# Kernel tuning notes

Hardware: AMD Instinct MI355X
Metric: run time of the kernel (lower is better)

Reference implementation:

```python
import jax, jax.numpy as jnp
import numpy as np

N, E, H, S = 50000, 400000, 128, 3  # nodes, edges, hidden_dim, mp steps
NODE_IN, EDGE_IN, OUT = 4, 3, 2


def _mlp(x, W1, b1, W2, b2, W3, b3):
    # MLP(in, [H, H], out): Linear->ReLU->Linear->ReLU->Linear
    h = jax.nn.relu(x @ W1 + b1)
    h = jax.nn.relu(h @ W2 + b2)
    return h @ W3 + b3


def setup_inputs() -> dict:
    key = jax.random.key(0)
    ks = iter(jax.random.split(key, 64))

    def p(shape):
        fan_in = shape[-2]
        return (jax.random.normal(next(ks), shape, jnp.float32) / np.float32(np.sqrt(fan_in)))

    inp = {}
    inp["x"] = jax.random.normal(next(ks), (N, NODE_IN), jnp.float32)
    inp["edge_attr"] = jax.random.normal(next(ks), (E, EDGE_IN), jnp.float32)
    inp["edge_index"] = jax.random.randint(next(ks), (2, E), 0, N, jnp.int32)
    # node encoder MLP(NODE_IN,[H,H],H)
    inp["ne_W1"], inp["ne_b1"] = p((NODE_IN, H)), jnp.zeros((H,), jnp.float32)
    inp["ne_W2"], inp["ne_b2"] = p((H, H)), jnp.zeros((H,), jnp.float32)
    inp["ne_W3"], inp["ne_b3"] = p((H, H)), jnp.zeros((H,), jnp.float32)
    # edge encoder MLP(EDGE_IN,[H,H],H)
    inp["ee_W1"], inp["ee_b1"] = p((EDGE_IN, H)), jnp.zeros((H,), jnp.float32)
    inp["ee_W2"], inp["ee_b2"] = p((H, H)), jnp.zeros((H,), jnp.float32)
    inp["ee_W3"], inp["ee_b3"] = p((H, H)), jnp.zeros((H,), jnp.float32)
    # processor: per-step edge MLP(3H,[H,H],H) and node MLP(2H,[H,H],H), stacked over S
    inp["pe_W1"], inp["pe_b1"] = p((S, 3 * H, H)), jnp.zeros((S, H), jnp.float32)
    inp["pe_W2"], inp["pe_b2"] = p((S, H, H)), jnp.zeros((S, H), jnp.float32)
    inp["pe_W3"], inp["pe_b3"] = p((S, H, H)), jnp.zeros((S, H), jnp.float32)
    inp["pn_W1"], inp["pn_b1"] = p((S, 2 * H, H)), jnp.zeros((S, H), jnp.float32)
    inp["pn_W2"], inp["pn_b2"] = p((S, H, H)), jnp.zeros((S, H), jnp.float32)
    inp["pn_W3"], inp["pn_b3"] = p((S, H, H)), jnp.zeros((S, H), jnp.float32)
    # node decoder MLP(H,[H,H],OUT)
    inp["nd_W1"], inp["nd_b1"] = p((H, H)), jnp.zeros((H,), jnp.float32)
    inp["nd_W2"], inp["nd_b2"] = p((H, H)), jnp.zeros((H,), jnp.float32)
    inp["nd_W3"], inp["nd_b3"] = p((H, OUT)), jnp.zeros((OUT,), jnp.float32)
    return inp


def reference(x, edge_attr, edge_index,
              ne_W1, ne_b1, ne_W2, ne_b2, ne_W3, ne_b3,
              ee_W1, ee_b1, ee_W2, ee_b2, ee_W3, ee_b3,
              pe_W1, pe_b1, pe_W2, pe_b2, pe_W3, pe_b3,
              pn_W1, pn_b1, pn_W2, pn_b2, pn_W3, pn_b3,
              nd_W1, nd_b1, nd_W2, nd_b2, nd_W3, nd_b3):
    src, dst = edge_index[0], edge_index[1]
    # encode
    h = _mlp(x, ne_W1, ne_b1, ne_W2, ne_b2, ne_W3, ne_b3)          # [N, H]
    e = _mlp(edge_attr, ee_W1, ee_b1, ee_W2, ee_b2, ee_W3, ee_b3)  # [E, H]
    # processor: gather -> edge MLP (residual) -> scatter-sum -> node MLP (residual)
    for t in range(S):
        m_in = jnp.concatenate([h[src], h[dst], e], axis=-1)        # [E, 3H]
        e = e + _mlp(m_in, pe_W1[t], pe_b1[t], pe_W2[t], pe_b2[t], pe_W3[t], pe_b3[t])
        agg = jax.ops.segment_sum(e, dst, num_segments=N)           # [N, H]
        n_in = jnp.concatenate([h, agg], axis=-1)                   # [N, 2H]
        h = h + _mlp(n_in, pn_W1[t], pn_b1[t], pn_W2[t], pn_b2[t], pn_W3[t], pn_b3[t])
    # decode
    return _mlp(h, nd_W1, nd_b1, nd_W2, nd_b2, nd_W3, nd_b3)        # [N, OUT]
```

## Files before the change

kernel.cpp:

```cpp
#include <hip/hip_runtime.h>
#include <hip/hip_bf16.h>
#include <cstddef>

#define NND 50000
#define NNDP 50048
#define NED 400000
#define HD 128
#define NSTEP 3
#define NSB 196
#define NWP 32

using u16 = unsigned short;
typedef __attribute__((ext_vector_type(8))) short bf16x8;
typedef __attribute__((ext_vector_type(4))) float f32x4;

__device__ __forceinline__ u16 f2b(float f) {
    __hip_bfloat16 b = __float2bfloat16(f);
    union { __hip_bfloat16 b; u16 u; } v; v.b = b;
    return v.u;
}
__device__ __forceinline__ float b2f(u16 u) {
    union { unsigned u; float f; } v; v.u = ((unsigned)u) << 16;
    return v.f;
}

template <int RT>
__device__ __forceinline__ void zero_accs(f32x4 (&acc)[RT][4]) {
    #pragma unroll
    for (int g = 0; g < RT; g++)
        #pragma unroll
        for (int i = 0; i < 4; i++) acc[g][i] = (f32x4)(0.0f);
}

__device__ __forceinline__ void mfma4T(bf16x8 act, const bf16x8 (&wf)[4], f32x4 (&accr)[4]) {
    accr[0] = __builtin_amdgcn_mfma_f32_16x16x32_bf16(wf[0], act, accr[0], 0, 0, 0);
    accr[1] = __builtin_amdgcn_mfma_f32_16x16x32_bf16(wf[1], act, accr[1], 0, 0, 0);
    accr[2] = __builtin_amdgcn_mfma_f32_16x16x32_bf16(wf[2], act, accr[2], 0, 0, 0);
    accr[3] = __builtin_amdgcn_mfma_f32_16x16x32_bf16(wf[3], act, accr[3], 0, 0, 0);
}

__device__ __forceinline__ void load_w16(const u16* __restrict__ Wf, int wc, int lane,
                                         bf16x8 (&wB)[16]) {
    const u16* bp = Wf + (size_t)(wc * 16) * 512 + lane * 8;
    #pragma unroll
    for (int i = 0; i < 16; i++) wB[i] = *(const bf16x8*)(bp + i * 512);
}

template <int RT>
__device__ __forceinline__ void gemm_reg_T(const u16* t, int rbase, const bf16x8 (&wB)[16],
                                           int lane, f32x4 (&acc)[RT][4]) {
    const int cl = lane & 15, q8 = (lane >> 4) * 8;
    #pragma unroll
    for (int k0 = 0; k0 < 4; k0++) {
        const bf16x8 wf[4] = {wB[k0], wB[4 + k0], wB[8 + k0], wB[12 + k0]};
        #pragma unroll
        for (int rt = 0; rt < RT; rt++) {
            bf16x8 a = *(const bf16x8*)(t + (rbase + rt * 16 + cl) * 136 + k0 * 32 + q8);
            mfma4T(a, wf, acc[rt]);
        }
    }
}

template <int KC, int RT>
__device__ __forceinline__ void gemm_lds_T(const u16* t, int rbase,
                                           const u16* __restrict__ Wf,
                                           int wc, int lane, f32x4 (&acc)[RT][4]) {
    const int cl = lane & 15, q8 = (lane >> 4) * 8;
    const u16* bp = Wf + (size_t)(wc * 4 * KC) * 512 + lane * 8;
    #pragma unroll
    for (int k0 = 0; k0 < KC; k0++) {
        bf16x8 wf[4];
        #pragma unroll
        for (int ct = 0; ct < 4; ct++) wf[ct] = *(const bf16x8*)(bp + (ct * KC + k0) * 512);
        #pragma unroll
        for (int rt = 0; rt < RT; rt++) {
            bf16x8 a = *(const bf16x8*)(t + (rbase + rt * 16 + cl) * 136 + k0 * 32 + q8);
            mfma4T(a, wf, acc[rt]);
        }
    }
}

template <int RT, bool RELU>
__device__ __forceinline__ void store_T(u16* T, int rbase, int wc, int lane,
        const f32x4 (&acc)[RT][4], const float* __restrict__ bias) {
    const int cl = lane & 15, q = lane >> 4;
    float4 bv[4];
    #pragma unroll
    for (int ct = 0; ct < 4; ct++)
        bv[ct] = *(const float4*)(bias + wc * 64 + ct * 16 + q * 4);
    #pragma unroll
    for (int rt = 0; rt < RT; rt++) {
        const int row = rbase + rt * 16 + cl;
        #pragma unroll
        for (int ct = 0; ct < 4; ct++) {
            float v0 = acc[rt][ct][0] + bv[ct].x;
            float v1 = acc[rt][ct][1] + bv[ct].y;
            float v2 = acc[rt][ct][2] + bv[ct].z;
            float v3 = acc[rt][ct][3] + bv[ct].w;
            if (RELU) {
                v0 = fmaxf(v0, 0.f); v1 = fmaxf(v1, 0.f);
                v2 = fmaxf(v2, 0.f); v3 = fmaxf(v3, 0.f);
            }
            uint2 pk;
            pk.x = (unsigned)f2b(v0) | ((unsigned)f2b(v1) << 16);
            pk.y = (unsigned)f2b(v2) | ((unsigned)f2b(v3) << 16);
            *(uint2*)(T + row * 136 + wc * 64 + ct * 16 + q * 4) = pk;
        }
    }
}

template <int RT>
__device__ __forceinline__ void store_T_nb(u16* T, int rbase, int wc, int lane,
        const f32x4 (&acc)[RT][4]) {
    const int cl = lane & 15, q = lane >> 4;
    #pragma unroll
    for (int rt = 0; rt < RT; rt++) {
        const int row = rbase + rt * 16 + cl;
        #pragma unroll
        for (int ct = 0; ct < 4; ct++) {
            uint2 pk;
            pk.x = (unsigned)f2b(acc[rt][ct][0]) | ((unsigned)f2b(acc[rt][ct][1]) << 16);
            pk.y = (unsigned)f2b(acc[rt][ct][2]) | ((unsigned)f2b(acc[rt][ct][3]) << 16);
            *(uint2*)(T + row * 136 + wc * 64 + ct * 16 + q * 4) = pk;
        }
    }
}

template <int RT>
__device__ __forceinline__ void epi_resid(const u16* T, u16* __restrict__ base, int row0,
        int rbase, int wc, int lane) {
    #pragma unroll
    for (int p = 0; p < RT * 2; p++) {
        const int lrow = rbase + p * 8 + (lane >> 3);
        const int col = wc * 64 + (lane & 7) * 8;
        bf16x8 tv = *(const bf16x8*)(T + lrow * 136 + col);
        u16* row = base + (size_t)(row0 + lrow) * HD + col;
        bf16x8 ov = *(const bf16x8*)row;
        bf16x8 res;
        #pragma unroll
        for (int k = 0; k < 8; k++)
            res[k] = (short)f2b(b2f((u16)tv[k]) + b2f((u16)ov[k]));
        *(bf16x8*)row = res;
    }
}

template <int RT>
__device__ __forceinline__ void epi_plain(const u16* T, u16* __restrict__ base, int row0,
        int rbase, int nrows, int wc, int lane) {
    #pragma unroll
    for (int p = 0; p < RT * 2; p++) {
        const int lrow = rbase + p * 8 + (lane >> 3);
        const int col = wc * 64 + (lane & 7) * 8;
        const int grow = row0 + lrow;
        if (grow < nrows) {
            bf16x8 tv = *(const bf16x8*)(T + lrow * 136 + col);
            *(bf16x8*)(base + (size_t)grow * HD + col) = tv;
        }
    }
}

__global__ void count_kernel(const int* __restrict__ eidx, int* __restrict__ counts) {
    int i = blockIdx.x * 256 + threadIdx.x;
    if (i < NED) atomicAdd(&counts[eidx[NED + i]], 1);
}

__global__ __launch_bounds__(256) void bsum_kernel(const int* __restrict__ counts,
                                                   int* __restrict__ bsum) {
    __shared__ int sm[256];
    const int i = threadIdx.x, b = blockIdx.x;
    const int idx = b * 256 + i;
    sm[i] = (idx < NNDP) ? counts[idx] : 0;
    __syncthreads();
    for (int ofs = 128; ofs > 0; ofs >>= 1) {
        if (i < ofs) sm[i] += sm[i + ofs];
        __syncthreads();
    }
    if (i == 0) bsum[b] = sm[0];
}

__global__ __launch_bounds__(256) void bscan_kernel(const int* __restrict__ bsum,
                                                    int* __restrict__ bbase,
                                                    int* __restrict__ offsets) {
    __shared__ int sm[256];
    const int i = threadIdx.x;
    int v = (i < NSB) ? bsum[i] : 0;
    sm[i] = v;
    __syncthreads();
    for (int ofs = 1; ofs < 256; ofs <<= 1) {
        int t = (i >= ofs) ? sm[i - ofs] : 0;
        __syncthreads();
        sm[i] += t;
        __syncthreads();
    }
    if (i < NSB) bbase[i] = sm[i] - v;
    if (i == NSB - 1) offsets[NNDP] = sm[i];
}

__global__ __launch_bounds__(256) void blocal_kernel(const int* __restrict__ counts,
                                                     const int* __restrict__ bbase,
                                                     int* __restrict__ offsets,
                                                     int* __restrict__ cursors) {
    __shared__ int sm[256];
    const int i = threadIdx.x, b = blockIdx.x;
    const int idx = b * 256 + i;
    int v = (idx < NNDP) ? counts[idx] : 0;
    sm[i] = v;
    __syncthreads();
    for (int ofs = 1; ofs < 256; ofs <<= 1) {
        int t = (i >= ofs) ? sm[i - ofs] : 0;
        __syncthreads();
        sm[i] += t;
        __syncthreads();
    }
    if (idx < NNDP) {
        int excl = sm[i] - v + bbase[b];
        offsets[idx] = excl;
        cursors[idx] = excl;
    }
}

__global__ void fill_kernel(const int* __restrict__ eidx, int* __restrict__ cursors,
                            int4* __restrict__ epk) {
    int i = blockIdx.x * 256 + threadIdx.x;
    if (i >= NED) return;
    int d = eidx[NED + i];
    int pos = atomicAdd(&cursors[d], 1);
    int4 v; v.x = eidx[i]; v.y = d; v.z = i; v.w = 0;
    epk[pos] = v;
}

struct WPall {
    const float* s[NWP];
    u16* d[NWP];
    int K[NWP];
    int Kp[NWP];
};

__global__ void wprep_all(WPall a) {
    const int wi = blockIdx.y;
    const int Kp = a.Kp[wi];
    int idx = blockIdx.x * 256 + threadIdx.x;
    if (idx >= 128 * Kp) return;
    const int K = a.K[wi];
    const float* __restrict__ src = a.s[wi];
    int j = idx & 7, lane = (idx >> 3) & 63, rest = idx >> 9;
    int KC = Kp >> 5;
    int k0 = rest % KC, n0 = rest / KC;
    int n = n0 * 16 + (lane & 15);
    int k = k0 * 32 + (lane >> 4) * 8 + j;
    float v = (k < K) ? src[(size_t)k * 128 + n] : 0.0f;
    a.d[wi][idx] = f2b(v);
}

__global__ __launch_bounds__(256, 2) void pnode_mfma(
    const u16* __restrict__ h,
    const u16* __restrict__ WsF, const u16* __restrict__ WdF,
    u16* __restrict__ Ps, u16* __restrict__ Pd) {
    __shared__ u16 t1[64 * 136];
    const int tid = threadIdx.x;
    const int lane = tid & 63, w = tid >> 6, wr = w >> 1, wc = w & 1;
    const int cl = lane & 15, q8 = (lane >> 4) * 8;
    const int row0 = blockIdx.x * 64;
    const int rbase = wr * 32;

    bf16x8 aA[2][4];
    #pragma unroll
    for (int rt = 0; rt < 2; rt++) {
        const u16* hp = h + (size_t)(row0 + rbase + rt * 16 + cl) * HD + q8;
        #pragma unroll
        for (int k0 = 0; k0 < 4; k0++) aA[rt][k0] = *(const bf16x8*)(hp + k0 * 32);
    }
    bf16x8 wB[16];
    f32x4 acc[2][4];

    load_w16(WsF, wc, lane, wB);
    zero_accs<2>(acc);
    #pragma unroll
    for (int k0 = 0; k0 < 4; k0++) {
        const bf16x8 wf[4] = {wB[k0], wB[4 + k0], wB[8 + k0], wB[12 + k0]};
        #pragma unroll
        for (int rt = 0; rt < 2; rt++) mfma4T(aA[rt][k0], wf, acc[rt]);
    }
    store_T_nb<2>(t1, rbase, wc, lane, acc);
    epi_plain<2>(t1, Ps, row0, rbase, NNDP, wc, lane);

    load_w16(WdF, wc, lane, wB);
    zero_accs<2>(acc);
    #pragma unroll
    for (int k0 = 0; k0 < 4; k0++) {
        const bf16x8 wf[4] = {wB[k0], wB[4 + k0], wB[8 + k0], wB[12 + k0]};
        #pragma unroll
        for (int rt = 0; rt < 2; rt++) mfma4T(aA[rt][k0], wf, acc[rt]);
    }
    store_T_nb<2>(t1, rbase, wc, lane, acc);
    epi_plain<2>(t1, Pd, row0, rbase, NNDP, wc, lane);
}

__global__ __launch_bounds__(256, 4) void enc_mfma(
    const float* __restrict__ in, int Kin, int nrows, const int4* __restrict__ epk,
    const u16* __restrict__ W1f, const float* __restrict__ b1,
    const u16* __restrict__ W2f, const float* __restrict__ b2,
    const u16* __restrict__ W3f, const float* __restrict__ b3,
    u16* __restrict__ out) {
    __shared__ u16 t1[64 * 136];
    __shared__ u16 t2[64 * 136];
    const int tid = threadIdx.x;
    const int lane = tid & 63, w = tid >> 6, wr = w >> 1, wc = w & 1;
    const int cl = lane & 15, q8 = (lane >> 4) * 8;
    const int row0 = blockIdx.x * 64;
    const int rbase = wr * 32;

    f32x4 acc[2][4];
    zero_accs<2>(acc);
    bf16x8 a[2];
    #pragma unroll
    for (int rt = 0; rt < 2; rt++) {
        a[rt] = (bf16x8){0, 0, 0, 0, 0, 0, 0, 0};
        int grow = row0 + rbase + rt * 16 + cl;
        if (q8 == 0 && grow < nrows) {
            int irow = epk ? epk[grow].z : grow;
            const float* xr = in + (size_t)irow * Kin;
            if (Kin == 4) {
                float4 v = *(const float4*)xr;
                a[rt][0] = (short)f2b(v.x); a[rt][1] = (short)f2b(v.y);
                a[rt][2] = (short)f2b(v.z); a[rt][3] = (short)f2b(v.w);
            } else {
                a[rt][0] = (short)f2b(xr[0]); a[rt][1] = (short)f2b(xr[1]);
                a[rt][2] = (short)f2b(xr[2]);
            }
        }
    }
    {
        const u16* b1p = W1f + (size_t)(wc * 4) * 512 + lane * 8;
        bf16x8 wf[4];
        #pragma unroll
        for (int ct = 0; ct < 4; ct++) wf[ct] = *(const bf16x8*)(b1p + ct * 512);
        #pragma unroll
        for (int rt = 0; rt < 2; rt++) mfma4T(a[rt], wf, acc[rt]);
    }
    store_T<2, true>(t1, rbase, wc, lane, acc, b1);
    __syncthreads();
    zero_accs<2>(acc);
    gemm_lds_T<4, 2>(t1, rbase, W2f, wc, lane, acc);
    store_T<2, true>(t2, rbase, wc, lane, acc, b2);
    __syncthreads();
    zero_accs<2>(acc);
    gemm_lds_T<4, 2>(t2, rbase, W3f, wc, lane, acc);
    store_T<2, false>(t1, rbase, wc, lane, acc, b3);
    epi_plain<2>(t1, out, row0, rbase, nrows, wc, lane);
}

__global__ __launch_bounds__(256, 2) void edge_mfma(
    u16* __restrict__ e, const int4* __restrict__ epk,
    const u16* __restrict__ Ps, const u16* __restrict__ Pd,
    const u16* __restrict__ W1eF, const float* __restrict__ b1,
    const u16* __restrict__ W2f, const float* __restrict__ b2,
    const u16* __restrict__ W3f, const float* __restrict__ b3) {
    __shared__ u16 t1[128 * 136];
    __shared__ u16 t2[128 * 136];
    const int tid = threadIdx.x;
    const int lane = tid & 63, w = tid >> 6, wr = w >> 1, wc = w & 1;
    const int cl = lane & 15, q = lane >> 4, q8 = q * 8;
    const int row0 = blockIdx.x * 128;
    const int rbase = wr * 64;

    bf16x8 wB[16];
    load_w16(W2f, wc, lane, wB);

    int srcv[4], dstv[4];
    const u16* epv[4];
    #pragma unroll
    for (int rt = 0; rt < 4; rt++) {
        int myrow = row0 + rbase + rt * 16 + cl;
        int4 pk = epk[myrow];
        srcv[rt] = pk.x; dstv[rt] = pk.y;
        epv[rt] = e + (size_t)myrow * HD + q8;
    }

    f32x4 acc[4][4];
    #pragma unroll
    for (int rt = 0; rt < 4; rt++) {
        const u16* ps = Ps + (size_t)srcv[rt] * HD + wc * 64 + q * 4;
        const u16* pd = Pd + (size_t)dstv[rt] * HD + wc * 64 + q * 4;
        #pragma unroll
        for (int ct = 0; ct < 4; ct++) {
            uint2 pa = *(const uint2*)(ps + ct * 16);
            uint2 pb = *(const uint2*)(pd + ct * 16);
            acc[rt][ct][0] = b2f((u16)(pa.x & 0xFFFF)) + b2f((u16)(pb.x & 0xFFFF));
            acc[rt][ct][1] = b2f((u16)(pa.x >> 16))    + b2f((u16)(pb.x >> 16));
            acc[rt][ct][2] = b2f((u16)(pa.y & 0xFFFF)) + b2f((u16)(pb.y & 0xFFFF));
            acc[rt][ct][3] = b2f((u16)(pa.y >> 16))    + b2f((u16)(pb.y >> 16));
        }
    }
    const u16* b1p = W1eF + (size_t)(wc * 16) * 512 + lane * 8;
    #pragma unroll
    for (int k0 = 0; k0 < 4; k0++) {
        bf16x8 wf[4];
        #pragma unroll
        for (int ct = 0; ct < 4; ct++) wf[ct] = *(const bf16x8*)(b1p + (ct * 4 + k0) * 512);
        #pragma unroll
        for (int rt = 0; rt < 4; rt++) {
            bf16x8 a = *(const bf16x8*)(epv[rt] + k0 * 32);
            mfma4T(a, wf, acc[rt]);
        }
    }
    store_T<4, true>(t1, rbase, wc, lane, acc, b1);
    __syncthreads();
    zero_accs<4>(acc);
    gemm_reg_T<4>(t1, rbase, wB, lane, acc);
    load_w16(W3f, wc, lane, wB);
    store_T<4, true>(t2, rbase, wc, lane, acc, b2);
    __syncthreads();
    zero_accs<4>(acc);
    gemm_reg_T<4>(t2, rbase, wB, lane, acc);
    store_T<4, false>(t1, rbase, wc, lane, acc, b3);
    epi_resid<4>(t1, e, row0, rbase, wc, lane);
}

__global__ __launch_bounds__(256, 4) void node_mfma(
    u16* __restrict__ h, const u16* __restrict__ e, const int* __restrict__ offsets,
    const u16* __restrict__ W1f, const float* __restrict__ b1,
    const u16* __restrict__ W2f, const float* __restrict__ b2,
    const u16* __restrict__ W3f, const float* __restrict__ b3) {
    __shared__ u16 tb[64 * 136];
    __shared__ u16 aggT[64 * 136];
    const int tid = threadIdx.x;
    const int lane = tid & 63, w = tid >> 6, wr = w >> 1, wc = w & 1;
    const int cl = lane & 15, q8 = (lane >> 4) * 8;
    const int row0 = blockIdx.x * 64;
    const int rbase = wr * 32;

    {
        const int r = tid >> 2, sgi = tid & 3;
        const int node = row0 + r;
        const int beg = offsets[node], end = offsets[node + 1];
        float s[32];
        #pragma unroll
        for (int k = 0; k < 32; k++) s[k] = 0.0f;
        const u16* ebase = e + sgi * 32;
        int j = beg;
        for (; j + 2 <= end; j += 2) {
            const bf16x8* e0 = (const bf16x8*)(ebase + (size_t)j * HD);
            const bf16x8* e1 = (const bf16x8*)(ebase + (size_t)(j + 1) * HD);
            bf16x8 v0 = e0[0], v1 = e0[1], v2 = e0[2], v3 = e0[3];
            bf16x8 u0 = e1[0], u1 = e1[1], u2 = e1[2], u3 = e1[3];
            #pragma unroll
            for (int k = 0; k < 8; k++) {
                s[k]      += b2f((u16)v0[k]) + b2f((u16)u0[k]);
                s[8 + k]  += b2f((u16)v1[k]) + b2f((u16)u1[k]);
                s[16 + k] += b2f((u16)v2[k]) + b2f((u16)u2[k]);
                s[24 + k] += b2f((u16)v3[k]) + b2f((u16)u3[k]);
            }
        }
        if (j < end) {
            const bf16x8* e0 = (const bf16x8*)(ebase + (size_t)j * HD);
            bf16x8 v0 = e0[0], v1 = e0[1], v2 = e0[2], v3 = e0[3];
            #pragma unroll
            for (int k = 0; k < 8; k++) {
                s[k]      += b2f((u16)v0[k]);
                s[8 + k]  += b2f((u16)v1[k]);
                s[16 + k] += b2f((u16)v2[k]);
                s[24 + k] += b2f((u16)v3[k]);
            }
        }
        #pragma unroll
        for (int q = 0; q < 4; q++) {
            bf16x8 o;
            #pragma unroll
            for (int k = 0; k < 8; k++) o[k] = (short)f2b(s[q * 8 + k]);
            *(bf16x8*)(aggT + r * 136 + sgi * 32 + q * 8) = o;
        }
    }
    __syncthreads();

    f32x4 acc[2][4];
    zero_accs<2>(acc);
    const u16* b1p = W1f + (size_t)(wc * 32) * 512 + lane * 8;
    const u16* hp[2];
    #pragma unroll
    for (int rt = 0; rt < 2; rt++)
        hp[rt] = h + (size_t)(row0 + rbase + rt * 16 + cl) * HD + q8;
    #pragma unroll
    for (int k0 = 0; k0 < 4; k0++) {
        bf16x8 wf[4];
        #pragma unroll
        for (int ct = 0; ct < 4; ct++) wf[ct] = *(const bf16x8*)(b1p + (ct * 8 + k0) * 512);
        #pragma unroll
        for (int rt = 0; rt < 2; rt++) {
            bf16x8 a = *(const bf16x8*)(hp[rt] + k0 * 32);
            mfma4T(a, wf, acc[rt]);
        }
    }
    #pragma unroll
    for (int k0 = 0; k0 < 4; k0++) {
        bf16x8 wf[4];
        #pragma unroll
        for (int ct = 0; ct < 4; ct++) wf[ct] = *(const bf16x8*)(b1p + (ct * 8 + 4 + k0) * 512);
        #pragma unroll
        for (int rt = 0; rt < 2; rt++) {
            bf16x8 a = *(const bf16x8*)(aggT + (rbase + rt * 16 + cl) * 136 + k0 * 32 + q8);
            mfma4T(a, wf, acc[rt]);
        }
    }
    store_T<2, true>(tb, rbase, wc, lane, acc, b1);
    __syncthreads();
    zero_accs<2>(acc);
    gemm_lds_T<4, 2>(tb, rbase, W2f, wc, lane, acc);
    store_T<2, true>(aggT, rbase, wc, lane, acc, b2);
    __syncthreads();
    zero_accs<2>(acc);
    gemm_lds_T<4, 2>(aggT, rbase, W3f, wc, lane, acc);
    store_T<2, false>(tb, rbase, wc, lane, acc, b3);
    epi_resid<2>(tb, h, row0, rbase, wc, lane);
}

__global__ __launch_bounds__(256, 4) void dec_mfma(
    const u16* __restrict__ h,
    const u16* __restrict__ W1f, const float* __restrict__ b1,
    const u16* __restrict__ W2f, const float* __restrict__ b2,
    const float* __restrict__ W3, const float* __restrict__ b3,
    float* __restrict__ out) {
    __shared__ u16 t1[32 * 136];
    __shared__ u16 t2[32 * 136];
    const int tid = threadIdx.x;
    const int lane = tid & 63, w = tid >> 6, wr = w >> 1, wc = w & 1;
    const int cl = lane & 15, q8 = (lane >> 4) * 8;
    const int row0 = blockIdx.x * 32;
    const int rbase = wr * 16;
    const u16* hp = h + (size_t)(row0 + rbase + cl) * HD + q8;

    f32x4 acc[1][4];
    zero_accs<1>(acc);
    const u16* b1p = W1f + (size_t)(wc * 16) * 512 + lane * 8;
    #pragma unroll
    for (int k0 = 0; k0 < 4; k0++) {
        bf16x8 wf[4];
        #pragma unroll
        for (int ct = 0; ct < 4; ct++) wf[ct] = *(const bf16x8*)(b1p + (ct * 4 + k0) * 512);
        bf16x8 a = *(const bf16x8*)(hp + k0 * 32);
        mfma4T(a, wf, acc[0]);
    }
    store_T<1, true>(t1, rbase, wc, lane, acc, b1);
    __syncthreads();
    zero_accs<1>(acc);
    gemm_lds_T<4, 1>(t1, rbase, W2f, wc, lane, acc);
    store_T<1, true>(t2, rbase, wc, lane, acc, b2);
    __syncthreads();
    if (tid < 64) {
        const int rr = tid >> 1, o = tid & 1;
        const int grow = row0 + rr;
        if (grow < NND) {
            float a = b3[o];
            for (int k = 0; k < HD; k++) a += b2f(t2[rr * 136 + k]) * W3[k * 2 + o];
            out[(size_t)grow * 2 + o] = a;
        }
    }
}

extern "C" void kernel_launch(void* const* d_in, const int* in_sizes, int n_in,
                              void* d_out, int out_size, void* d_ws, size_t ws_size,
                              hipStream_t stream) {
    (void)in_sizes; (void)n_in; (void)out_size; (void)ws_size;
    const float* x    = (const float*)d_in[0];
    const float* eatt = (const float*)d_in[1];
    const int*   eidx = (const int*)d_in[2];
    const float *neW1 = (const float*)d_in[3],  *neb1 = (const float*)d_in[4];
    const float *neW2 = (const float*)d_in[5],  *neb2 = (const float*)d_in[6];
    const float *neW3 = (const float*)d_in[7],  *neb3 = (const float*)d_in[8];
    const float *eeW1 = (const float*)d_in[9],  *eeb1 = (const float*)d_in[10];
    const float *eeW2 = (const float*)d_in[11], *eeb2 = (const float*)d_in[12];
    const float *eeW3 = (const float*)d_in[13], *eeb3 = (const float*)d_in[14];
    const float *peW1 = (const float*)d_in[15], *peb1 = (const float*)d_in[16];
    const float *peW2 = (const float*)d_in[17], *peb2 = (const float*)d_in[18];
    const float *peW3 = (const float*)d_in[19], *peb3 = (const float*)d_in[20];
    const float *pnW1 = (const float*)d_in[21], *pnb1 = (const float*)d_in[22];
    const float *pnW2 = (const float*)d_in[23], *pnb2 = (const float*)d_in[24];
    const float *pnW3 = (const float*)d_in[25], *pnb3 = (const float*)d_in[26];
    const float *ndW1 = (const float*)d_in[27], *ndb1 = (const float*)d_in[28];
    const float *ndW2 = (const float*)d_in[29], *ndb2 = (const float*)d_in[30];
    const float *ndW3 = (const float*)d_in[31], *ndb3 = (const float*)d_in[32];

    char* ws = (char*)d_ws;
    u16*   h       = (u16*)ws;
    u16*   e       = (u16*)(ws + 12812288);
    int*   bsum    = (int*)(ws + 115212288);
    int*   bbase   = (int*)(ws + 115213312);
    int*   counts  = (int*)(ws + 115245056);
    int*   cursors = (int*)(ws + 115445248);
    int*   offsets = (int*)(ws + 115645440);
    int4*  epk     = (int4*)(ws + 115845760);
    u16*   Ps      = (u16*)(ws + 122245760);
    u16*   Pd      = (u16*)(ws + 135058048);
    u16*   wts     = (u16*)(ws + 147870336);

    u16* p = wts;
    u16 *neW1t = p; p += 128 * 32;
    u16 *neW2t = p; p += 128 * 128;
    u16 *neW3t = p; p += 128 * 128;
    u16 *eeW1t = p; p += 128 * 32;
    u16 *eeW2t = p; p += 128 * 128;
    u16 *eeW3t = p; p += 128 * 128;
    u16 *peW1sF[NSTEP], *peW1dF[NSTEP], *peW1eF[NSTEP], *peW2t[NSTEP], *peW3t[NSTEP];
    u16 *pnW1t[NSTEP], *pnW2t[NSTEP], *pnW3t[NSTEP];
    for (int t = 0; t < NSTEP; t++) {
        peW1sF[t] = p; p += 128 * 128;
        peW1dF[t] = p; p += 128 * 128;
        peW1eF[t] = p; p += 128 * 128;
        peW2t[t]  = p; p += 128 * 128;
        peW3t[t]  = p; p += 128 * 128;
    }
    for (int t = 0; t < NSTEP; t++) {
        pnW1t[t] = p; p += 128 * 256;
        pnW2t[t] = p; p += 128 * 128;
        pnW3t[t] = p; p += 128 * 128;
    }
    u16 *ndW1t = p; p += 128 * 128;
    u16 *ndW2t = p; p += 128 * 128;

    hipMemsetAsync(counts, 0, NNDP * sizeof(int), stream);
    count_kernel<<<(NED + 255) / 256, 256, 0, stream>>>(eidx, counts);
    bsum_kernel<<<NSB, 256, 0, stream>>>(counts, bsum);
    bscan_kernel<<<1, 256, 0, stream>>>(bsum, bbase, offsets);
    blocal_kernel<<<NSB, 256, 0, stream>>>(counts, bbase, offsets, cursors);
    fill_kernel<<<(NED + 255) / 256, 256, 0, stream>>>(eidx, cursors, epk);

    WPall wa;
    int wn = 0;
    auto ADD = [&](const float* s, u16* d, int K, int Kp) {
        wa.s[wn] = s; wa.d[wn] = d; wa.K[wn] = K; wa.Kp[wn] = Kp; wn++;
    };
    ADD(neW1, neW1t, 4, 32);
    ADD(neW2, neW2t, 128, 128);
    ADD(neW3, neW3t, 128, 128);
    ADD(eeW1, eeW1t, 3, 32);
    ADD(eeW2, eeW2t, 128, 128);
    ADD(eeW3, eeW3t, 128, 128);
    for (int t = 0; t < NSTEP; t++) {
        const float* base = peW1 + (size_t)t * 384 * 128;
        ADD(base,             peW1sF[t], 128, 128);
        ADD(base + 128 * 128, peW1dF[t], 128, 128);
        ADD(base + 256 * 128, peW1eF[t], 128, 128);
        ADD(peW2 + (size_t)t * 128 * 128, peW2t[t], 128, 128);
        ADD(peW3 + (size_t)t * 128 * 128, peW3t[t], 128, 128);
        ADD(pnW1 + (size_t)t * 256 * 128, pnW1t[t], 256, 256);
        ADD(pnW2 + (size_t)t * 128 * 128, pnW2t[t], 128, 128);
        ADD(pnW3 + (size_t)t * 128 * 128, pnW3t[t], 128, 128);
    }
    ADD(ndW1, ndW1t, 128, 128);
    ADD(ndW2, ndW2t, 128, 128);
    wprep_all<<<dim3(128, NWP), 256, 0, stream>>>(wa);

    enc_mfma<<<NNDP / 64, 256, 0, stream>>>(x, 4, NND, nullptr,
                                            neW1t, neb1, neW2t, neb2, neW3t, neb3, h);
    enc_mfma<<<NED / 64, 256, 0, stream>>>(eatt, 3, NED, epk,
                                           eeW1t, eeb1, eeW2t, eeb2, eeW3t, eeb3, e);
    pnode_mfma<<<NNDP / 64, 256, 0, stream>>>(h, peW1sF[0], peW1dF[0], Ps, Pd);

    for (int t = 0; t < NSTEP; t++) {
        edge_mfma<<<NED / 128, 256, 0, stream>>>(
            e, epk, Ps, Pd,
            peW1eF[t], peb1 + (size_t)t * HD,
            peW2t[t],  peb2 + (size_t)t * HD,
            peW3t[t],  peb3 + (size_t)t * HD);
        node_mfma<<<NNDP / 64, 256, 0, stream>>>(
            h, e, offsets,
            pnW1t[t], pnb1 + (size_t)t * HD,
            pnW2t[t], pnb2 + (size_t)t * HD,
            pnW3t[t], pnb3 + (size_t)t * HD);
        if (t + 1 < NSTEP)
            pnode_mfma<<<NNDP / 64, 256, 0, stream>>>(h, peW1sF[t + 1], peW1dF[t + 1], Ps, Pd);
    }
    dec_mfma<<<NNDP / 32, 256, 0, stream>>>(h, ndW1t, ndb1, ndW2t, ndb2, ndW3, ndb3, (float*)d_out);
}
```

Baseline: 566.4 us.

## Fuse next-step node projections into node kernel and permute P layout for wide gathers

The separate pnode_mfma launch between steps is removed: node_mfma now computes the updated h, keeps it in LDS, and immediately projects it with the next step's src/dst weights into Ps/Pd. The Ps/Pd row layout is permuted so the edge kernel can gather each lane's values with two 16-byte loads instead of four 8-byte loads per row. Residual operands (old e and h) are prefetched into registers before the final GEMM to hide global latency. The cost is higher register pressure (node kernel launch bounds drop to 3 blocks per CU) and a longer node kernel.

Measured after the change: 531.3 us. 1.07x faster.

```diff
diff --git a/kernel.cpp b/kernel.cpp
--- a/kernel.cpp
+++ b/kernel.cpp
@@ -110,7 +110,7 @@
 }
 
 template <int RT>
-__device__ __forceinline__ void store_T_nb(u16* T, int rbase, int wc, int lane,
+__device__ __forceinline__ void store_T_perm(u16* T, int rbase, int wc, int lane,
         const f32x4 (&acc)[RT][4]) {
     const int cl = lane & 15, q = lane >> 4;
     #pragma unroll
@@ -121,26 +121,8 @@
             uint2 pk;
             pk.x = (unsigned)f2b(acc[rt][ct][0]) | ((unsigned)f2b(acc[rt][ct][1]) << 16);
             pk.y = (unsigned)f2b(acc[rt][ct][2]) | ((unsigned)f2b(acc[rt][ct][3]) << 16);
-            *(uint2*)(T + row * 136 + wc * 64 + ct * 16 + q * 4) = pk;
-        }
-    }
-}
-
-template <int RT>
-__device__ __forceinline__ void epi_resid(const u16* T, u16* __restrict__ base, int row0,
-        int rbase, int wc, int lane) {
-    #pragma unroll
-    for (int p = 0; p < RT * 2; p++) {
-        const int lrow = rbase + p * 8 + (lane >> 3);
-        const int col = wc * 64 + (lane & 7) * 8;
-        bf16x8 tv = *(const bf16x8*)(T + lrow * 136 + col);
-        u16* row = base + (size_t)(row0 + lrow) * HD + col;
-        bf16x8 ov = *(const bf16x8*)row;
-        bf16x8 res;
-        #pragma unroll
-        for (int k = 0; k < 8; k++)
-            res[k] = (short)f2b(b2f((u16)tv[k]) + b2f((u16)ov[k]));
-        *(bf16x8*)row = res;
+            *(uint2*)(T + row * 136 + wc * 64 + q * 16 + ct * 4) = pk;
+        }
     }
 }
 
@@ -281,7 +263,7 @@
         #pragma unroll
         for (int rt = 0; rt < 2; rt++) mfma4T(aA[rt][k0], wf, acc[rt]);
     }
-    store_T_nb<2>(t1, rbase, wc, lane, acc);
+    store_T_perm<2>(t1, rbase, wc, lane, acc);
     epi_plain<2>(t1, Ps, row0, rbase, NNDP, wc, lane);
 
     load_w16(WdF, wc, lane, wB);
@@ -292,7 +274,7 @@
         #pragma unroll
         for (int rt = 0; rt < 2; rt++) mfma4T(aA[rt][k0], wf, acc[rt]);
     }
-    store_T_nb<2>(t1, rbase, wc, lane, acc);
+    store_T_perm<2>(t1, rbase, wc, lane, acc);
     epi_plain<2>(t1, Pd, row0, rbase, NNDP, wc, lane);
 }
 
@@ -377,20 +359,26 @@
         epv[rt] = e + (size_t)myrow * HD + q8;
     }
 
+    const int pofs = wc * 64 + q * 16;
     f32x4 acc[4][4];
     #pragma unroll
     for (int rt = 0; rt < 4; rt++) {
-        const u16* ps = Ps + (size_t)srcv[rt] * HD + wc * 64 + q * 4;
-        const u16* pd = Pd + (size_t)dstv[rt] * HD + wc * 64 + q * 4;
-        #pragma unroll
-        for (int ct = 0; ct < 4; ct++) {
-            uint2 pa = *(const uint2*)(ps + ct * 16);
-            uint2 pb = *(const uint2*)(pd + ct * 16);
-            acc[rt][ct][0] = b2f((u16)(pa.x & 0xFFFF)) + b2f((u16)(pb.x & 0xFFFF));
-            acc[rt][ct][1] = b2f((u16)(pa.x >> 16))    + b2f((u16)(pb.x >> 16));
-            acc[rt][ct][2] = b2f((u16)(pa.y & 0xFFFF)) + b2f((u16)(pb.y & 0xFFFF));
-            acc[rt][ct][3] = b2f((u16)(pa.y >> 16))    + b2f((u16)(pb.y >> 16));
-        }
+        const u16* ps = Ps + (size_t)srcv[rt] * HD + pofs;
+        const u16* pd = Pd + (size_t)dstv[rt] * HD + pofs;
+        bf16x8 a0 = *(const bf16x8*)ps;
+        bf16x8 a1 = *(const bf16x8*)(ps + 8);
+        bf16x8 b0 = *(const bf16x8*)pd;
+        bf16x8 b1v = *(const bf16x8*)(pd + 8);
+        #pragma unroll
+        for (int ct = 0; ct < 2; ct++)
+            #pragma unroll
+            for (int i = 0; i < 4; i++)
+                acc[rt][ct][i] = b2f((u16)a0[ct * 4 + i]) + b2f((u16)b0[ct * 4 + i]);
+        #pragma unroll
+        for (int ct = 2; ct < 4; ct++)
+            #pragma unroll
+            for (int i = 0; i < 4; i++)
+                acc[rt][ct][i] = b2f((u16)a1[(ct - 2) * 4 + i]) + b2f((u16)b1v[(ct - 2) * 4 + i]);
     }
     const u16* b1p = W1eF + (size_t)(wc * 16) * 512 + lane * 8;
     #pragma unroll
@@ -411,17 +399,36 @@
     load_w16(W3f, wc, lane, wB);
     store_T<4, true>(t2, rbase, wc, lane, acc, b2);
     __syncthreads();
+    bf16x8 eold[8];
+    #pragma unroll
+    for (int p = 0; p < 8; p++) {
+        const int lrow = rbase + p * 8 + (lane >> 3);
+        const int col = wc * 64 + (lane & 7) * 8;
+        eold[p] = *(const bf16x8*)(e + (size_t)(row0 + lrow) * HD + col);
+    }
     zero_accs<4>(acc);
     gemm_reg_T<4>(t2, rbase, wB, lane, acc);
     store_T<4, false>(t1, rbase, wc, lane, acc, b3);
-    epi_resid<4>(t1, e, row0, rbase, wc, lane);
-}
-
-__global__ __launch_bounds__(256, 4) void node_mfma(
+    #pragma unroll
+    for (int p = 0; p < 8; p++) {
+        const int lrow = rbase + p * 8 + (lane >> 3);
+        const int col = wc * 64 + (lane & 7) * 8;
+        bf16x8 tv = *(const bf16x8*)(t1 + lrow * 136 + col);
+        bf16x8 res;
+        #pragma unroll
+        for (int k = 0; k < 8; k++)
+            res[k] = (short)f2b(b2f((u16)tv[k]) + b2f((u16)eold[p][k]));
+        *(bf16x8*)(e + (size_t)(row0 + lrow) * HD + col) = res;
+    }
+}
+
+__global__ __launch_bounds__(256, 3) void node_mfma(
     u16* __restrict__ h, const u16* __restrict__ e, const int* __restrict__ offsets,
     const u16* __restrict__ W1f, const float* __restrict__ b1,
     const u16* __restrict__ W2f, const float* __restrict__ b2,
-    const u16* __restrict__ W3f, const float* __restrict__ b3) {
+    const u16* __restrict__ W3f, const float* __restrict__ b3,
+    const u16* __restrict__ W1sNx, const u16* __restrict__ W1dNx,
+    u16* __restrict__ Ps, u16* __restrict__ Pd) {
     __shared__ u16 tb[64 * 136];
     __shared__ u16 aggT[64 * 136];
     const int tid = threadIdx.x;
@@ -508,10 +515,43 @@
     gemm_lds_T<4, 2>(tb, rbase, W2f, wc, lane, acc);
     store_T<2, true>(aggT, rbase, wc, lane, acc, b2);
     __syncthreads();
+    bf16x8 hold[4];
+    #pragma unroll
+    for (int p = 0; p < 4; p++) {
+        const int lrow = rbase + p * 8 + (lane >> 3);
+        const int col = wc * 64 + (lane & 7) * 8;
+        hold[p] = *(const bf16x8*)(h + (size_t)(row0 + lrow) * HD + col);
+    }
     zero_accs<2>(acc);
     gemm_lds_T<4, 2>(aggT, rbase, W3f, wc, lane, acc);
     store_T<2, false>(tb, rbase, wc, lane, acc, b3);
-    epi_resid<2>(tb, h, row0, rbase, wc, lane);
+    #pragma unroll
+    for (int p = 0; p < 4; p++) {
+        const int lrow = rbase + p * 8 + (lane >> 3);
+        const int col = wc * 64 + (lane & 7) * 8;
+        bf16x8 tv = *(const bf16x8*)(tb + lrow * 136 + col);
+        bf16x8 res;
+        #pragma unroll
+        for (int k = 0; k < 8; k++)
+            res[k] = (short)f2b(b2f((u16)tv[k]) + b2f((u16)hold[p][k]));
+        *(bf16x8*)(h + (size_t)(row0 + lrow) * HD + col) = res;
+        *(bf16x8*)(tb + lrow * 136 + col) = res;
+    }
+    if (W1sNx) {
+        __syncthreads();
+        bf16x8 wB[16];
+        load_w16(W1sNx, wc, lane, wB);
+        f32x4 pac[2][4];
+        zero_accs<2>(pac);
+        gemm_reg_T<2>(tb, rbase, wB, lane, pac);
+        store_T_perm<2>(aggT, rbase, wc, lane, pac);
+        epi_plain<2>(aggT, Ps, row0, rbase, NNDP, wc, lane);
+        load_w16(W1dNx, wc, lane, wB);
+        zero_accs<2>(pac);
+        gemm_reg_T<2>(tb, rbase, wB, lane, pac);
+        store_T_perm<2>(aggT, rbase, wc, lane, pac);
+        epi_plain<2>(aggT, Pd, row0, rbase, NNDP, wc, lane);
+    }
 }
 
 __global__ __launch_bounds__(256, 4) void dec_mfma(
@@ -662,13 +702,15 @@
             peW1eF[t], peb1 + (size_t)t * HD,
             peW2t[t],  peb2 + (size_t)t * HD,
             peW3t[t],  peb3 + (size_t)t * HD);
+        const bool last = (t + 1 == NSTEP);
         node_mfma<<<NNDP / 64, 256, 0, stream>>>(
             h, e, offsets,
             pnW1t[t], pnb1 + (size_t)t * HD,
             pnW2t[t], pnb2 + (size_t)t * HD,
-            pnW3t[t], pnb3 + (size_t)t * HD);
-        if (t + 1 < NSTEP)
-            pnode_mfma<<<NNDP / 64, 256, 0, stream>>>(h, peW1sF[t + 1], peW1dF[t + 1], Ps, Pd);
+            pnW3t[t], pnb3 + (size_t)t * HD,
+            last ? nullptr : peW1sF[t + 1],
+            last ? nullptr : peW1dF[t + 1],
+            Ps, Pd);
     }
     dec_mfma<<<NNDP / 32, 256, 0, stream>>>(h, ndW1t, ndb1, ndW2t, ndb2, ndW3, ndb3, (float*)d_out);
 }
```
